# Optimization experiments

Measured on AMD Instinct MI355X. Metric: run time of the kernel, lower is better.

Reference implementation:

```python
import jax, jax.numpy as jnp
import numpy as np

B, S, D, H, HD = 4, 2048, 2048, 16, 128
NEG_INF = -1e10


def setup_inputs() -> dict:
    key = jax.random.key(0)
    ks = jax.random.split(key, 7)
    scale = 1.0 / np.sqrt(D)  # variance_scaling(1.0, 'fan_in') approx
    inputs_q = jax.random.normal(ks[0], (B, S, D), jnp.float32)
    inputs_kv = jax.random.normal(ks[1], (B, S, D), jnp.float32)
    mask = jax.random.randint(ks[2], (B, 1, S, S), 0, 2, jnp.int32)
    Wq = jax.random.normal(ks[3], (D, H, HD), jnp.float32) * scale
    Wk = jax.random.normal(ks[4], (D, H, HD), jnp.float32) * scale
    Wv = jax.random.normal(ks[5], (D, H, HD), jnp.float32) * scale
    Wo = jax.random.normal(ks[6], (H, HD, D), jnp.float32) * (1.0 / np.sqrt(H * HD))
    return {"inputs_q": inputs_q, "inputs_kv": inputs_kv, "mask": mask,
            "Wq": Wq, "Wk": Wk, "Wv": Wv, "Wo": Wo}


def reference(inputs_q, inputs_kv, mask, Wq, Wk, Wv, Wo):
    # QKV projections: [B,S,D] x [D,H,HD] -> [B,S,H,HD]
    q = jnp.einsum('bsd,dhk->bshk', inputs_q, Wq)
    k = jnp.einsum('bsd,dhk->bshk', inputs_kv, Wk)
    v = jnp.einsum('bsd,dhk->bshk', inputs_kv, Wv)
    # mask -> additive bias: 0 where mask>0, else -1e10
    attn_bias = jnp.where(mask > 0, 0.0, NEG_INF).astype(q.dtype)  # [B,1,S,S]
    # scaled dot-product attention
    q = q / jnp.sqrt(jnp.asarray(HD, q.dtype))
    logits = jnp.einsum('bqhd,bkhd->bhqk', q, k) + attn_bias  # [B,H,S,S]
    weights = jax.nn.softmax(logits, axis=-1)
    x = jnp.einsum('bhqk,bkhd->bqhd', weights, v)  # [B,S,H,HD]
    # out projection contracts (heads, head_dim) -> embed
    out = jnp.einsum('bqhd,hdo->bqo', x, Wo)  # [B,S,D]
    return out
```

## Files before the change

kernel.cpp:

```cpp
#include <hip/hip_runtime.h>

typedef __attribute__((ext_vector_type(4))) float f32x4;
typedef __attribute__((ext_vector_type(8))) short bf16x8;
typedef unsigned int uint;
typedef unsigned short ushort;

#define mfma32 __builtin_amdgcn_mfma_f32_16x16x32_bf16


__device__ __forceinline__ ushort f2bf(float f) {
  union { float f; uint u; } v; v.f = f;
  uint u = v.u;
  uint r = (u + 0x7FFFu + ((u >> 16) & 1u)) >> 16;
  return (ushort)r;
}
__device__ __forceinline__ float bf2f(ushort u) {
  union { uint u; float f; } v; v.u = ((uint)u) << 16;
  return v.f;
}

__device__ __forceinline__ uint cvt_pk_bf16(float lo, float hi) {
  uint r;
  asm("v_cvt_pk_bf16_f32 %0, %1, %2" : "=v"(r) : "v"(lo), "v"(hi));
  return r;
}

__device__ __forceinline__ float fexp2(float x) {
  float r;
  asm("v_exp_f32 %0, %1" : "=v"(r) : "v"(x));
  return r;
}

__device__ __forceinline__ void gload_lds16(const void* g, void* l) {
  __builtin_amdgcn_global_load_lds(
      (const __attribute__((address_space(1))) void*)g,
      (__attribute__((address_space(3))) void*)l, 16, 0, 0);
}


__global__ __launch_bounds__(256)
void conv_bf16_2(const float* __restrict__ a, const float* __restrict__ b,
                 ushort* __restrict__ oa, ushort* __restrict__ ob, long n) {
  const bool second = blockIdx.x >= 8192;
  const float* in = second ? b : a;
  ushort* out = second ? ob : oa;
  long i = ((long)(blockIdx.x & 8191) * 256 + threadIdx.x) * 8;
  if (i >= n) return;
  float4 x = *(const float4*)(in + i);
  float4 y = *(const float4*)(in + i + 4);
  union { uint u[4]; uint4 v; } o;
  o.u[0] = cvt_pk_bf16(x.x, x.y);
  o.u[1] = cvt_pk_bf16(x.z, x.w);
  o.u[2] = cvt_pk_bf16(y.x, y.y);
  o.u[3] = cvt_pk_bf16(y.z, y.w);
  *(uint4*)(out + i) = o.v;
}


__global__ __launch_bounds__(256)
void transpose64f(const float* p0, const float* p1, const float* p2, const float* p3,
                  ushort* q0, ushort* q1, ushort* q2, ushort* q3, int R, int C) {
  __shared__ float tile[64][68];
  const int z = blockIdx.z;
  const float* in = z == 0 ? p0 : z == 1 ? p1 : z == 2 ? p2 : p3;
  ushort* out = z == 0 ? q0 : z == 1 ? q1 : z == 2 ? q2 : q3;
  const int r0 = blockIdx.y * 64, c0 = blockIdx.x * 64;
  const int tid = threadIdx.x;
#pragma unroll
  for (int j = 0; j < 4; ++j) {
    int flat = j * 256 + tid;
    int row = flat >> 4, c4 = (flat & 15) * 4;
    float4 v = *(const float4*)(in + (size_t)(r0 + row) * C + c0 + c4);
    *(float4*)&tile[row][c4] = v;
  }
  __syncthreads();
#pragma unroll
  for (int j = 0; j < 4; ++j) {
    int flat = j * 256 + tid;
    int oc = flat >> 4, rq = (flat & 15) * 4;
    uint2 w;
    w.x = cvt_pk_bf16(tile[rq + 0][oc], tile[rq + 1][oc]);
    w.y = cvt_pk_bf16(tile[rq + 2][oc], tile[rq + 3][oc]);
    *(uint2*)(out + (size_t)(c0 + oc) * R + r0 + rq) = w;
  }
}

__global__ __launch_bounds__(256)
void transpose64h(const ushort* p0, const ushort* p1, const ushort* p2, const ushort* p3,
                  ushort* q0, ushort* q1, ushort* q2, ushort* q3, int R, int C) {
  __shared__ float tile[64][68];
  const int z = blockIdx.z;
  const ushort* in = z == 0 ? p0 : z == 1 ? p1 : z == 2 ? p2 : p3;
  ushort* out = z == 0 ? q0 : z == 1 ? q1 : z == 2 ? q2 : q3;
  const int r0 = blockIdx.y * 64, c0 = blockIdx.x * 64;
  const int tid = threadIdx.x;
#pragma unroll
  for (int j = 0; j < 2; ++j) {
    int flat = j * 256 + tid;
    int row = flat >> 3, c8 = (flat & 7) * 8;
    uint4 v = *(const uint4*)(in + (size_t)(r0 + row) * C + c0 + c8);
    float4 f0, f1;
    f0.x = bf2f((ushort)(v.x & 0xffff)); f0.y = bf2f((ushort)(v.x >> 16));
    f0.z = bf2f((ushort)(v.y & 0xffff)); f0.w = bf2f((ushort)(v.y >> 16));
    f1.x = bf2f((ushort)(v.z & 0xffff)); f1.y = bf2f((ushort)(v.z >> 16));
    f1.z = bf2f((ushort)(v.w & 0xffff)); f1.w = bf2f((ushort)(v.w >> 16));
    *(float4*)&tile[row][c8] = f0;
    *(float4*)&tile[row][c8 + 4] = f1;
  }
  __syncthreads();
#pragma unroll
  for (int j = 0; j < 4; ++j) {
    int flat = j * 256 + tid;
    int oc = flat >> 4, rq = (flat & 15) * 4;
    uint2 w;
    w.x = cvt_pk_bf16(tile[rq + 0][oc], tile[rq + 1][oc]);
    w.y = cvt_pk_bf16(tile[rq + 2][oc], tile[rq + 3][oc]);
    *(uint2*)(out + (size_t)(c0 + oc) * R + r0 + rq) = w;
  }
}

__global__ __launch_bounds__(256)
void pack_mask(const int* __restrict__ in, uint* __restrict__ out) {
  long t = (long)blockIdx.x * 256 + threadIdx.x;
  const int4* p = (const int4*)(in + t * 32);
  uint w = 0;
#pragma unroll
  for (int i = 0; i < 8; ++i) {
    int4 v = p[i];
    w |= (v.x > 0 ? 1u : 0u) << (i * 4 + 0);
    w |= (v.y > 0 ? 1u : 0u) << (i * 4 + 1);
    w |= (v.z > 0 ? 1u : 0u) << (i * 4 + 2);
    w |= (v.w > 0 ? 1u : 0u) << (i * 4 + 3);
  }
  out[t] = w;
}


template<int OUT_BF16>
__global__ __launch_bounds__(512, 2)
void gemm256(const ushort* __restrict__ A, const ushort* __restrict__ Bt,
             void* __restrict__ C, int M, int N, int K, float scale) {
  __shared__ ushort lA[2][256 * 64];
  __shared__ ushort lB[2][256 * 64];
  const int tid = threadIdx.x;
  const int wid = tid >> 6, lane = tid & 63;
  const int lg = lane >> 4, li = lane & 15;
  const int wm = wid >> 2, wn = wid & 3;
  const int m0 = blockIdx.y * 256, n0 = blockIdx.x * 256;

  int offA[4], offB[4];
#pragma unroll
  for (int i = 0; i < 4; ++i) {
    int off = i * 8192 + tid * 16;
    int row = off >> 7;
    int col = (off & 127) ^ ((row & 7) << 4);
    offA[i] = (m0 + row) * (K * 2) + col;
    offB[i] = (n0 + row) * (K * 2) + col;
  }
  const char* Ab = (const char*)A;
  const char* Bb = (const char*)Bt;

#define STAGE256(bufi, ktb)                                                   \
  do {                                                                        \
    _Pragma("unroll") for (int i = 0; i < 4; ++i)                             \
      gload_lds16(Ab + (size_t)(offA[i] + (ktb)),                             \
                  (char*)lA[bufi] + i * 8192 + wid * 1024);                   \
    _Pragma("unroll") for (int i = 0; i < 4; ++i)                             \
      gload_lds16(Bb + (size_t)(offB[i] + (ktb)),                             \
                  (char*)lB[bufi] + i * 8192 + wid * 1024);                   \
  } while (0)

  f32x4 acc[8][4] = {};
  const int NT = K >> 6;

  STAGE256(0, 0);

  for (int t = 0; t < NT; ++t) {
    const int cur = t & 1;
    if (t > 0) __builtin_amdgcn_s_barrier();
    if (t + 1 < NT) {
      STAGE256(cur ^ 1, (t + 1) * 128);
      asm volatile("s_waitcnt vmcnt(8)" ::: "memory");
    } else {
      asm volatile("s_waitcnt vmcnt(0)" ::: "memory");
    }
    __builtin_amdgcn_s_barrier();
    __builtin_amdgcn_sched_barrier(0);

    const char* la = (const char*)lA[cur];
    const char* lb = (const char*)lB[cur];

    bf16x8 bfr[4][2];
#pragma unroll
    for (int ni = 0; ni < 4; ++ni)
#pragma unroll
      for (int ks = 0; ks < 2; ++ks) {
        const int row = wn * 64 + ni * 16 + li;
        bfr[ni][ks] = *(const bf16x8*)(
            lb + row * 128 + ((ks * 64 + lg * 16) ^ ((li & 7) << 4)));
      }

    bf16x8 afr[4][2];
#pragma unroll
    for (int mh = 0; mh < 2; ++mh) {
#pragma unroll
      for (int mi = 0; mi < 4; ++mi)
#pragma unroll
        for (int ks = 0; ks < 2; ++ks) {
          const int row = wm * 128 + (mh * 4 + mi) * 16 + li;
          afr[mi][ks] = *(const bf16x8*)(
              la + row * 128 + ((ks * 64 + lg * 16) ^ ((li & 7) << 4)));
        }
      __builtin_amdgcn_s_setprio(1);
#pragma unroll
      for (int ks = 0; ks < 2; ++ks)
#pragma unroll
        for (int mi = 0; mi < 4; ++mi)
#pragma unroll
          for (int ni = 0; ni < 4; ++ni)
            acc[mh * 4 + mi][ni] = mfma32(
                afr[mi][ks], bfr[ni][ks], acc[mh * 4 + mi][ni], 0, 0, 0);
      __builtin_amdgcn_s_setprio(0);
    }
  }
#undef STAGE256

  const int r0 = m0 + wm * 128 + lg * 4;
  const int c0 = n0 + wn * 64 + li;
#pragma unroll
  for (int mi = 0; mi < 8; ++mi)
#pragma unroll
    for (int ni = 0; ni < 4; ++ni)
#pragma unroll
      for (int r = 0; r < 4; ++r) {
        size_t idx = (size_t)(r0 + mi * 16 + r) * N + (c0 + ni * 16);
        float v = acc[mi][ni][r] * scale;
        if (OUT_BF16) ((ushort*)C)[idx] = f2bf(v);
        else          ((float*)C)[idx]  = v;
      }
}


__global__ __launch_bounds__(256, 2)
void flash_attn6(const ushort* __restrict__ Q, const ushort* __restrict__ K,
                 const ushort* __restrict__ VT, const uint* __restrict__ maskp,
                 ushort* __restrict__ X) {
  __shared__ ushort lK[2][64 * 128];
  __shared__ ushort lVT[2][128 * 64];
  __shared__ ushort lP[4][2][16 * 64];

  const int tid = threadIdx.x;
  const int wid = tid >> 6;
  const int lane = tid & 63;
  const int lg = lane >> 4, li = lane & 15;

  const int flat = blockIdx.x;
  const int xcd = flat & 7;
  const int j = flat >> 3;
  const int bh = xcd * 8 + (j >> 4);
  const int qt = j & 15;
  const int b = bh >> 4, h = bh & 15;
  const int q0 = qt * 128;
  const int qbase = q0 + wid * 32;

  bf16x8 bq[2][4];
#pragma unroll
  for (int g = 0; g < 2; ++g) {
    const ushort* qrow = Q + (size_t)(b * 2048 + qbase + g * 16 + li) * 2048 + h * 128;
#pragma unroll
    for (int kk = 0; kk < 4; ++kk)
      bq[g][kk] = *(const bf16x8*)(qrow + kk * 32 + lg * 8);
  }

  const uint* mqb[2] = {
      maskp + (size_t)(b * 2048 + qbase + li) * 64,
      maskp + (size_t)(b * 2048 + qbase + 16 + li) * 64};
  uint2 wcur[2] = {*(const uint2*)mqb[0], *(const uint2*)mqb[1]};

  f32x4 acc_o[2][8] = {};
  f32x4 acc_l[2] = {};
  float m[2] = {-3e38f, -3e38f};

  const short ob = (short)0x3F80;
  const bf16x8 vone8 = {ob, ob, ob, ob, ob, ob, ob, ob};

  const char* gk[4];
  const char* gv[4];
#pragma unroll
  for (int i = 0; i < 4; ++i) {
    int fl = i * 4096 + tid * 16;
    int rowK = fl >> 8;
    int colK = (fl & 255) ^ ((rowK & 15) << 4);
    gk[i] = (const char*)K + ((size_t)(b * 2048 + rowK) * 2048 + h * 128) * 2 + colK;
    int rowV = fl >> 7;
    int colV = (fl & 127) ^ ((rowV & 7) << 4);
    gv[i] = (const char*)VT + ((size_t)((b * 16 + h) * 128 + rowV) * 2048) * 2 + colV;
  }

#define FSTAGE(bufi)                                                          \
  do {                                                                        \
    _Pragma("unroll") for (int i = 0; i < 4; ++i)                             \
      gload_lds16(gk[i], (char*)lK[bufi] + i * 4096 + wid * 1024);            \
    _Pragma("unroll") for (int i = 0; i < 4; ++i)                             \
      gload_lds16(gv[i], (char*)lVT[bufi] + i * 4096 + wid * 1024);           \
    _Pragma("unroll") for (int i = 0; i < 4; ++i) {                           \
      gk[i] += 262144; gv[i] += 128;                                          \
    }                                                                         \
  } while (0)

  FSTAGE(0);

  ushort* lp0 = lP[wid][0];
  ushort* lp1 = lP[wid][1];

#pragma unroll 2
  for (int it = 0; it < 32; ++it) {
    const int cur = it & 1;
    if (it > 0) __builtin_amdgcn_s_barrier();
    uint2 wn[2];
    if (it < 31) {
      FSTAGE(cur ^ 1);
      wn[0] = *(const uint2*)(mqb[0] + (it + 1) * 2);
      wn[1] = *(const uint2*)(mqb[1] + (it + 1) * 2);
      asm volatile("s_waitcnt vmcnt(10)" ::: "memory");
    } else {
      asm volatile("s_waitcnt vmcnt(0)" ::: "memory");
    }
    __builtin_amdgcn_s_barrier();
    __builtin_amdgcn_sched_barrier(0);

    const char* lk = (const char*)lK[cur];
    const char* lv = (const char*)lVT[cur];

    f32x4 accs[2][4] = {};
    __builtin_amdgcn_s_setprio(1);
#pragma unroll
    for (int kk = 0; kk < 4; ++kk)
#pragma unroll
      for (int n = 0; n < 4; ++n) {
        bf16x8 ak = *(const bf16x8*)(lk + (n * 16 + li) * 256 +
                                     ((kk * 64 + lg * 16) ^ (li << 4)));
        accs[0][n] = mfma32(ak, bq[0][kk], accs[0][n], 0, 0, 0);
        accs[1][n] = mfma32(ak, bq[1][kk], accs[1][n], 0, 0, 0);
      }
    __builtin_amdgcn_s_setprio(0);

#pragma unroll
    for (int g = 0; g < 2; ++g) {
      float sv[16];
#pragma unroll
      for (int n = 0; n < 4; ++n) {
        uint w = (n < 2) ? wcur[g].x : wcur[g].y;
#pragma unroll
        for (int r = 0; r < 4; ++r) {
          int bit = (n & 1) * 16 + lg * 4 + r;
          sv[n * 4 + r] = ((w >> bit) & 1u) ? accs[g][n][r] : -1e10f;
        }
      }
      float t0 = fmaxf(fmaxf(sv[0], sv[1]), sv[2]);
      float t1 = fmaxf(fmaxf(sv[3], sv[4]), sv[5]);
      float t2 = fmaxf(fmaxf(sv[6], sv[7]), sv[8]);
      float t3 = fmaxf(fmaxf(sv[9], sv[10]), sv[11]);
      float t4 = fmaxf(fmaxf(sv[12], sv[13]), sv[14]);
      float pmax = fmaxf(fmaxf(fmaxf(t0, t1), t2),
                         fmaxf(fmaxf(t3, t4), sv[15]));
      pmax = fmaxf(pmax, __shfl_xor(pmax, 16, 64));
      pmax = fmaxf(pmax, __shfl_xor(pmax, 32, 64));

      if (!__all(pmax - m[g] <= 11.5f)) {
        float mnew = fmaxf(m[g], pmax);
        float alpha = fexp2(m[g] - mnew);
#pragma unroll
        for (int r = 0; r < 4; ++r) acc_l[g][r] *= alpha;
#pragma unroll
        for (int f = 0; f < 8; ++f)
#pragma unroll
          for (int r = 0; r < 4; ++r) acc_o[g][f][r] *= alpha;
        m[g] = mnew;
      }

      uint pk[8];
#pragma unroll
      for (int i = 0; i < 8; ++i) {
        float p0 = fexp2(sv[2 * i] - m[g]);
        float p1 = fexp2(sv[2 * i + 1] - m[g]);
        pk[i] = cvt_pk_bf16(p0, p1);
      }

      ushort* lpg = g ? lp1 : lp0;
#pragma unroll
      for (int n = 0; n < 4; ++n) {
        uint2 pw; pw.x = pk[2 * n]; pw.y = pk[2 * n + 1];
        *(uint2*)((char*)lpg + li * 128 + ((n * 32 + lg * 8) ^ ((li & 7) << 4))) = pw;
      }
    }

    __builtin_amdgcn_s_setprio(1);
#pragma unroll
    for (int kc = 0; kc < 2; ++kc) {
      bf16x8 bp0 = *(const bf16x8*)((const char*)lp0 + li * 128 +
                                    ((kc * 64 + lg * 16) ^ ((li & 7) << 4)));
      bf16x8 bp1 = *(const bf16x8*)((const char*)lp1 + li * 128 +
                                    ((kc * 64 + lg * 16) ^ ((li & 7) << 4)));
      acc_l[0] = mfma32(vone8, bp0, acc_l[0], 0, 0, 0);
      acc_l[1] = mfma32(vone8, bp1, acc_l[1], 0, 0, 0);
#pragma unroll
      for (int f = 0; f < 8; ++f) {
        bf16x8 av = *(const bf16x8*)(lv + (f * 16 + li) * 128 +
                                     ((kc * 64 + lg * 16) ^ ((li & 7) << 4)));
        acc_o[0][f] = mfma32(av, bp0, acc_o[0][f], 0, 0, 0);
        acc_o[1][f] = mfma32(av, bp1, acc_o[1][f], 0, 0, 0);
      }
    }
    __builtin_amdgcn_s_setprio(0);

    if (it < 31) { wcur[0] = wn[0]; wcur[1] = wn[1]; }
  }
#undef FSTAGE

#pragma unroll
  for (int g = 0; g < 2; ++g) {
    const float inv_l = 1.0f / acc_l[g][0];
    ushort* xrow = X + (size_t)(b * 2048 + qbase + g * 16 + li) * 2048 + h * 128;
#pragma unroll
    for (int f = 0; f < 8; ++f) {
      union { ushort u[4]; uint2 v; } o;
#pragma unroll
      for (int r = 0; r < 4; ++r) o.u[r] = f2bf(acc_o[g][f][r] * inv_l);
      *(uint2*)(xrow + f * 16 + lg * 4) = o.v;
    }
  }
}


extern "C" void kernel_launch(void* const* d_in, const int* in_sizes, int n_in,
                              void* d_out, int out_size, void* d_ws, size_t ws_size,
                              hipStream_t stream) {
  const float* inputs_q  = (const float*)d_in[0];
  const float* inputs_kv = (const float*)d_in[1];
  const int*   mask      = (const int*)d_in[2];
  const float* Wq        = (const float*)d_in[3];
  const float* Wk        = (const float*)d_in[4];
  const float* Wv        = (const float*)d_in[5];
  const float* Wo        = (const float*)d_in[6];
  float* out = (float*)d_out;
  char* ws = (char*)d_ws;

  uint*   maskp = (uint*)(ws + 0);
  ushort* xq    = (ushort*)(ws + 2097152);
  ushort* xkv   = (ushort*)(ws + 35651584);
  ushort* WqT   = (ushort*)(ws + 69206016);
  ushort* WkT   = (ushort*)(ws + 77594624);
  ushort* WvT   = (ushort*)(ws + 85983232);
  ushort* WoT   = (ushort*)(ws + 94371840);
  ushort* Qb    = (ushort*)(ws + 102760448);
  ushort* Kb    = (ushort*)(ws + 136314880);
  ushort* Vb    = (ushort*)(ws + 169869312);
  ushort* VTb   = xq;
  ushort* Xb    = xkv;

  const long NE = 8192L * 2048;
  conv_bf16_2<<<16384, 256, 0, stream>>>(inputs_q, inputs_kv, xq, xkv, NE);

  transpose64f<<<dim3(32, 32, 4), 256, 0, stream>>>(
      Wq, Wk, Wv, Wo, WqT, WkT, WvT, WoT, 2048, 2048);

  pack_mask<<<2048, 256, 0, stream>>>(mask, maskp);

  const float qscale = 0.12751744504593677f;
  gemm256<1><<<dim3(8, 32), 512, 0, stream>>>(xq,  WqT, Qb, 8192, 2048, 2048, qscale);
  gemm256<1><<<dim3(8, 32), 512, 0, stream>>>(xkv, WkT, Kb, 8192, 2048, 2048, 1.0f);
  gemm256<1><<<dim3(8, 32), 512, 0, stream>>>(xkv, WvT, Vb, 8192, 2048, 2048, 1.0f);

  const long BS = 2048L * 2048;
  transpose64h<<<dim3(32, 32, 4), 256, 0, stream>>>(
      Vb, Vb + BS, Vb + 2 * BS, Vb + 3 * BS,
      VTb, VTb + BS, VTb + 2 * BS, VTb + 3 * BS, 2048, 2048);

  flash_attn6<<<1024, 256, 0, stream>>>(Qb, Kb, VTb, maskp, Xb);

  gemm256<0><<<dim3(8, 32), 512, 0, stream>>>(Xb, WoT, out, 8192, 2048, 2048, 1.0f);
}
```

Before: 569.3 us.

## Fuse V transpose into GEMM epilogue and merge prepass kernels

The V projection GEMM gains an output mode that writes bf16 results directly in transposed [B, HD*H, S] layout. This removes the separate V buffer and the transpose64h pass that re-read and re-wrote it. The fp32→bf16 input conversion, the weight transposes and the mask bit-packing are merged into one prepass launch, cutting launch overhead. The flash attention loop now waits for all outstanding loads and barriers before issuing the next K/V prefetch, which is simpler but may expose more load latency. The transposed epilogue stores are 8-byte strided writes, which coalesce less well than row-major stores.

```diff
diff --git a/kernel.cpp b/kernel.cpp
--- a/kernel.cpp
+++ b/kernel.cpp
@@ -14,10 +14,6 @@
   uint r = (u + 0x7FFFu + ((u >> 16) & 1u)) >> 16;
   return (ushort)r;
 }
-__device__ __forceinline__ float bf2f(ushort u) {
-  union { uint u; float f; } v; v.u = ((uint)u) << 16;
-  return v.f;
-}
 
 __device__ __forceinline__ uint cvt_pk_bf16(float lo, float hi) {
   uint r;
@@ -39,104 +35,72 @@
 
 
 __global__ __launch_bounds__(256)
-void conv_bf16_2(const float* __restrict__ a, const float* __restrict__ b,
-                 ushort* __restrict__ oa, ushort* __restrict__ ob, long n) {
-  const bool second = blockIdx.x >= 8192;
-  const float* in = second ? b : a;
-  ushort* out = second ? ob : oa;
-  long i = ((long)(blockIdx.x & 8191) * 256 + threadIdx.x) * 8;
-  if (i >= n) return;
-  float4 x = *(const float4*)(in + i);
-  float4 y = *(const float4*)(in + i + 4);
-  union { uint u[4]; uint4 v; } o;
-  o.u[0] = cvt_pk_bf16(x.x, x.y);
-  o.u[1] = cvt_pk_bf16(x.z, x.w);
-  o.u[2] = cvt_pk_bf16(y.x, y.y);
-  o.u[3] = cvt_pk_bf16(y.z, y.w);
-  *(uint4*)(out + i) = o.v;
-}
-
-
-__global__ __launch_bounds__(256)
-void transpose64f(const float* p0, const float* p1, const float* p2, const float* p3,
-                  ushort* q0, ushort* q1, ushort* q2, ushort* q3, int R, int C) {
+void prepass(const float* __restrict__ iq, const float* __restrict__ ikv,
+             ushort* __restrict__ xq, ushort* __restrict__ xkv,
+             const float* __restrict__ Wq, const float* __restrict__ Wk,
+             const float* __restrict__ Wv, const float* __restrict__ Wo,
+             ushort* __restrict__ WqT, ushort* __restrict__ WkT,
+             ushort* __restrict__ WvT, ushort* __restrict__ WoT,
+             const int* __restrict__ mask, uint* __restrict__ maskp) {
   __shared__ float tile[64][68];
-  const int z = blockIdx.z;
-  const float* in = z == 0 ? p0 : z == 1 ? p1 : z == 2 ? p2 : p3;
-  ushort* out = z == 0 ? q0 : z == 1 ? q1 : z == 2 ? q2 : q3;
-  const int r0 = blockIdx.y * 64, c0 = blockIdx.x * 64;
+  const int bid = blockIdx.x;
   const int tid = threadIdx.x;
-#pragma unroll
-  for (int j = 0; j < 4; ++j) {
-    int flat = j * 256 + tid;
-    int row = flat >> 4, c4 = (flat & 15) * 4;
-    float4 v = *(const float4*)(in + (size_t)(r0 + row) * C + c0 + c4);
-    *(float4*)&tile[row][c4] = v;
-  }
-  __syncthreads();
-#pragma unroll
-  for (int j = 0; j < 4; ++j) {
-    int flat = j * 256 + tid;
-    int oc = flat >> 4, rq = (flat & 15) * 4;
-    uint2 w;
-    w.x = cvt_pk_bf16(tile[rq + 0][oc], tile[rq + 1][oc]);
-    w.y = cvt_pk_bf16(tile[rq + 2][oc], tile[rq + 3][oc]);
-    *(uint2*)(out + (size_t)(c0 + oc) * R + r0 + rq) = w;
-  }
-}
-
-__global__ __launch_bounds__(256)
-void transpose64h(const ushort* p0, const ushort* p1, const ushort* p2, const ushort* p3,
-                  ushort* q0, ushort* q1, ushort* q2, ushort* q3, int R, int C) {
-  __shared__ float tile[64][68];
-  const int z = blockIdx.z;
-  const ushort* in = z == 0 ? p0 : z == 1 ? p1 : z == 2 ? p2 : p3;
-  ushort* out = z == 0 ? q0 : z == 1 ? q1 : z == 2 ? q2 : q3;
-  const int r0 = blockIdx.y * 64, c0 = blockIdx.x * 64;
-  const int tid = threadIdx.x;
-#pragma unroll
-  for (int j = 0; j < 2; ++j) {
-    int flat = j * 256 + tid;
-    int row = flat >> 3, c8 = (flat & 7) * 8;
-    uint4 v = *(const uint4*)(in + (size_t)(r0 + row) * C + c0 + c8);
-    float4 f0, f1;
-    f0.x = bf2f((ushort)(v.x & 0xffff)); f0.y = bf2f((ushort)(v.x >> 16));
-    f0.z = bf2f((ushort)(v.y & 0xffff)); f0.w = bf2f((ushort)(v.y >> 16));
-    f1.x = bf2f((ushort)(v.z & 0xffff)); f1.y = bf2f((ushort)(v.z >> 16));
-    f1.z = bf2f((ushort)(v.w & 0xffff)); f1.w = bf2f((ushort)(v.w >> 16));
-    *(float4*)&tile[row][c8] = f0;
-    *(float4*)&tile[row][c8 + 4] = f1;
-  }
-  __syncthreads();
-#pragma unroll
-  for (int j = 0; j < 4; ++j) {
-    int flat = j * 256 + tid;
-    int oc = flat >> 4, rq = (flat & 15) * 4;
-    uint2 w;
-    w.x = cvt_pk_bf16(tile[rq + 0][oc], tile[rq + 1][oc]);
-    w.y = cvt_pk_bf16(tile[rq + 2][oc], tile[rq + 3][oc]);
-    *(uint2*)(out + (size_t)(c0 + oc) * R + r0 + rq) = w;
-  }
-}
-
-__global__ __launch_bounds__(256)
-void pack_mask(const int* __restrict__ in, uint* __restrict__ out) {
-  long t = (long)blockIdx.x * 256 + threadIdx.x;
-  const int4* p = (const int4*)(in + t * 32);
-  uint w = 0;
-#pragma unroll
-  for (int i = 0; i < 8; ++i) {
-    int4 v = p[i];
-    w |= (v.x > 0 ? 1u : 0u) << (i * 4 + 0);
-    w |= (v.y > 0 ? 1u : 0u) << (i * 4 + 1);
-    w |= (v.z > 0 ? 1u : 0u) << (i * 4 + 2);
-    w |= (v.w > 0 ? 1u : 0u) << (i * 4 + 3);
-  }
-  out[t] = w;
-}
-
-
-template<int OUT_BF16>
+
+  if (bid < 16384) {
+    const bool second = bid >= 8192;
+    const float* in = second ? ikv : iq;
+    ushort* out = second ? xkv : xq;
+    long i = ((long)(bid & 8191) * 256 + tid) * 8;
+    float4 x = *(const float4*)(in + i);
+    float4 y = *(const float4*)(in + i + 4);
+    union { uint u[4]; uint4 v; } o;
+    o.u[0] = cvt_pk_bf16(x.x, x.y);
+    o.u[1] = cvt_pk_bf16(x.z, x.w);
+    o.u[2] = cvt_pk_bf16(y.x, y.y);
+    o.u[3] = cvt_pk_bf16(y.z, y.w);
+    *(uint4*)(out + i) = o.v;
+  } else if (bid < 20480) {
+    const int t = bid - 16384;
+    const int z = t >> 10;
+    const int by = (t >> 5) & 31, bx = t & 31;
+    const float* in = z == 0 ? Wq : z == 1 ? Wk : z == 2 ? Wv : Wo;
+    ushort* out = z == 0 ? WqT : z == 1 ? WkT : z == 2 ? WvT : WoT;
+    const int r0 = by * 64, c0 = bx * 64;
+#pragma unroll
+    for (int j = 0; j < 4; ++j) {
+      int flat = j * 256 + tid;
+      int row = flat >> 4, c4 = (flat & 15) * 4;
+      float4 v = *(const float4*)(in + (size_t)(r0 + row) * 2048 + c0 + c4);
+      *(float4*)&tile[row][c4] = v;
+    }
+    __syncthreads();
+#pragma unroll
+    for (int j = 0; j < 4; ++j) {
+      int flat = j * 256 + tid;
+      int oc = flat >> 4, rq = (flat & 15) * 4;
+      uint2 w;
+      w.x = cvt_pk_bf16(tile[rq + 0][oc], tile[rq + 1][oc]);
+      w.y = cvt_pk_bf16(tile[rq + 2][oc], tile[rq + 3][oc]);
+      *(uint2*)(out + (size_t)(c0 + oc) * 2048 + r0 + rq) = w;
+    }
+  } else {
+    long t = (long)(bid - 20480) * 256 + tid;
+    const int4* p = (const int4*)(mask + t * 32);
+    uint w = 0;
+#pragma unroll
+    for (int i = 0; i < 8; ++i) {
+      int4 v = p[i];
+      w |= (v.x > 0 ? 1u : 0u) << (i * 4 + 0);
+      w |= (v.y > 0 ? 1u : 0u) << (i * 4 + 1);
+      w |= (v.z > 0 ? 1u : 0u) << (i * 4 + 2);
+      w |= (v.w > 0 ? 1u : 0u) << (i * 4 + 3);
+    }
+    maskp[t] = w;
+  }
+}
+
+
+template<int OUT_MODE>
 __global__ __launch_bounds__(512, 2)
 void gemm256(const ushort* __restrict__ A, const ushort* __restrict__ Bt,
              void* __restrict__ C, int M, int N, int K, float scale) {
@@ -227,17 +191,33 @@
 
   const int r0 = m0 + wm * 128 + lg * 4;
   const int c0 = n0 + wn * 64 + li;
-#pragma unroll
-  for (int mi = 0; mi < 8; ++mi)
-#pragma unroll
-    for (int ni = 0; ni < 4; ++ni)
-#pragma unroll
-      for (int r = 0; r < 4; ++r) {
-        size_t idx = (size_t)(r0 + mi * 16 + r) * N + (c0 + ni * 16);
-        float v = acc[mi][ni][r] * scale;
-        if (OUT_BF16) ((ushort*)C)[idx] = f2bf(v);
-        else          ((float*)C)[idx]  = v;
-      }
+  if constexpr (OUT_MODE == 2) {
+    const int b_ = r0 >> 11;
+    const int s0 = r0 & 2047;
+    ushort* VT = (ushort*)C;
+#pragma unroll
+    for (int mi = 0; mi < 8; ++mi)
+#pragma unroll
+      for (int ni = 0; ni < 4; ++ni) {
+        union { ushort u[4]; uint2 v; } o;
+#pragma unroll
+        for (int r = 0; r < 4; ++r) o.u[r] = f2bf(acc[mi][ni][r] * scale);
+        *(uint2*)(VT + ((size_t)(b_ * 2048 + c0 + ni * 16)) * 2048 +
+                  s0 + mi * 16) = o.v;
+      }
+  } else {
+#pragma unroll
+    for (int mi = 0; mi < 8; ++mi)
+#pragma unroll
+      for (int ni = 0; ni < 4; ++ni)
+#pragma unroll
+        for (int r = 0; r < 4; ++r) {
+          size_t idx = (size_t)(r0 + mi * 16 + r) * N + (c0 + ni * 16);
+          float v = acc[mi][ni][r] * scale;
+          if (OUT_MODE == 1) ((ushort*)C)[idx] = f2bf(v);
+          else               ((float*)C)[idx]  = v;
+        }
+  }
 }
 
 
@@ -316,18 +296,16 @@
 #pragma unroll 2
   for (int it = 0; it < 32; ++it) {
     const int cur = it & 1;
-    if (it > 0) __builtin_amdgcn_s_barrier();
+    asm volatile("s_waitcnt vmcnt(0)" ::: "memory");
+    __builtin_amdgcn_s_barrier();
+    __builtin_amdgcn_sched_barrier(0);
+
     uint2 wn[2];
     if (it < 31) {
       FSTAGE(cur ^ 1);
       wn[0] = *(const uint2*)(mqb[0] + (it + 1) * 2);
       wn[1] = *(const uint2*)(mqb[1] + (it + 1) * 2);
-      asm volatile("s_waitcnt vmcnt(10)" ::: "memory");
-    } else {
-      asm volatile("s_waitcnt vmcnt(0)" ::: "memory");
-    }
-    __builtin_amdgcn_s_barrier();
-    __builtin_amdgcn_sched_barrier(0);
+    }
 
     const char* lk = (const char*)lK[cur];
     const char* lv = (const char*)lVT[cur];
@@ -455,27 +433,17 @@
   ushort* WoT   = (ushort*)(ws + 94371840);
   ushort* Qb    = (ushort*)(ws + 102760448);
   ushort* Kb    = (ushort*)(ws + 136314880);
-  ushort* Vb    = (ushort*)(ws + 169869312);
   ushort* VTb   = xq;
   ushort* Xb    = xkv;
 
-  const long NE = 8192L * 2048;
-  conv_bf16_2<<<16384, 256, 0, stream>>>(inputs_q, inputs_kv, xq, xkv, NE);
-
-  transpose64f<<<dim3(32, 32, 4), 256, 0, stream>>>(
-      Wq, Wk, Wv, Wo, WqT, WkT, WvT, WoT, 2048, 2048);
-
-  pack_mask<<<2048, 256, 0, stream>>>(mask, maskp);
+  prepass<<<22528, 256, 0, stream>>>(inputs_q, inputs_kv, xq, xkv,
+                                     Wq, Wk, Wv, Wo, WqT, WkT, WvT, WoT,
+                                     mask, maskp);
 
   const float qscale = 0.12751744504593677f;
   gemm256<1><<<dim3(8, 32), 512, 0, stream>>>(xq,  WqT, Qb, 8192, 2048, 2048, qscale);
   gemm256<1><<<dim3(8, 32), 512, 0, stream>>>(xkv, WkT, Kb, 8192, 2048, 2048, 1.0f);
-  gemm256<1><<<dim3(8, 32), 512, 0, stream>>>(xkv, WvT, Vb, 8192, 2048, 2048, 1.0f);
-
-  const long BS = 2048L * 2048;
-  transpose64h<<<dim3(32, 32, 4), 256, 0, stream>>>(
-      Vb, Vb + BS, Vb + 2 * BS, Vb + 3 * BS,
-      VTb, VTb + BS, VTb + 2 * BS, VTb + 3 * BS, 2048, 2048);
+  gemm256<2><<<dim3(8, 32), 512, 0, stream>>>(xkv, WvT, VTb, 8192, 2048, 2048, 1.0f);
 
   flash_attn6<<<1024, 256, 0, stream>>>(Qb, Kb, VTb, maskp, Xb);
 
```

Measured after the change: 544.9 us. 4.3% less time.
